# Performance work log

Measured on AMD Instinct MI355X. Metric: run time of the kernel, lower is better.

The kernel has to match this reference:

```python
import jax, jax.numpy as jnp
from jax import lax
import numpy as np

B, W, V, E, H = 512, 40, 12000, 512, 512


def setup_inputs() -> dict:
    key = jax.random.key(0)
    ks = jax.random.split(key, 9)
    s = 0.05
    ques_vec = jax.random.randint(ks[0], (B, W), 0, V + 1)          # token ids, 0 = pad
    ques_len = jax.random.randint(ks[1], (B,), 1, W + 1)             # valid lengths in [1, W]
    lookup_W = jax.random.normal(ks[2], (E, V), jnp.float32) * s     # nn.Linear(vocab, emb).weight
    wih0 = jax.random.normal(ks[3], (2, 4 * H, E), jnp.float32) * s  # [dir, 4H, in]
    whh0 = jax.random.normal(ks[4], (2, 4 * H, H), jnp.float32) * s
    b0 = jax.random.normal(ks[5], (2, 2, 4 * H), jnp.float32) * s    # [dir, {b_ih,b_hh}, 4H]
    wih1 = jax.random.normal(ks[6], (2, 4 * H, 2 * H), jnp.float32) * s
    whh1 = jax.random.normal(ks[7], (2, 4 * H, H), jnp.float32) * s
    b1 = jax.random.normal(ks[8], (2, 2, 4 * H), jnp.float32) * s
    return {"ques_vec": ques_vec, "ques_len": ques_len, "lookup_W": lookup_W,
            "wih0": wih0, "whh0": whh0, "b0": b0,
            "wih1": wih1, "whh1": whh1, "b1": b1}


def _lstm_dir(x, wih, whh, b, reverse):
    # x: [B, T, D]; PyTorch gate order i, f, g, o
    Hc = whh.shape[1]
    xg = jnp.einsum('btd,gd->btg', x, wih) + b[0] + b[1]  # [B, T, 4H]
    xs = jnp.swapaxes(xg, 0, 1)                            # [T, B, 4H]
    if reverse:
        xs = xs[::-1]

    def step(carry, g_t):
        h, c = carry
        g = g_t + h @ whh.T
        i, f, gg, o = jnp.split(g, 4, axis=-1)
        c = jax.nn.sigmoid(f) * c + jax.nn.sigmoid(i) * jnp.tanh(gg)
        h = jax.nn.sigmoid(o) * jnp.tanh(c)
        return (h, c), h

    h0 = jnp.zeros((x.shape[0], Hc), x.dtype)
    _, hs = lax.scan(step, (h0, h0), xs)
    if reverse:
        hs = hs[::-1]
    return jnp.swapaxes(hs, 0, 1)  # [B, T, H]


def _bilstm(x, wih, whh, b):
    fwd = _lstm_dir(x, wih[0], whh[0], b[0], False)
    bwd = _lstm_dir(x, wih[1], whh[1], b[1], True)
    return jnp.concatenate([fwd, bwd], axis=-1)  # [B, T, 2H]


def reference(ques_vec, ques_len, lookup_W, wih0, whh0, b0, wih1, whh1, b1):
    # one-hot over vocab+1 with column 0 dropped == gather with id 0 -> zero vector
    table = jnp.concatenate([jnp.zeros((1, E), lookup_W.dtype), lookup_W.T], axis=0)  # [V+1, E]
    emb = jnp.tanh(table[ques_vec])          # [B, W, E] (dropout=0 -> identity)
    h = _bilstm(emb, wih0, whh0, b0)         # layer 0
    h = _bilstm(h, wih1, whh1, b1)           # layer 1 -> [B, W, 2H]
    # scatter-mask bmm == select hidden state at timestep ques_len-1
    idx = (ques_len - 1)[:, None, None]
    return jnp.take_along_axis(h, idx, axis=1).reshape(ques_vec.shape[0], -1)  # [B, 2H]
```

## Files before the change

### kernel.cpp

```cpp
#include <hip/hip_runtime.h>
#include <hip/hip_bf16.h>
#include <stdint.h>

#define NB 512
#define NW 40
#define NE 512
#define NH 512
#define NV 12000
#define G4 2048

typedef unsigned short u16;
typedef unsigned int u32;
typedef unsigned long long u64;
typedef __attribute__((ext_vector_type(8))) short short8;
typedef __attribute__((ext_vector_type(4))) float f32x4;

__device__ __forceinline__ unsigned short f2bf(float f) {
  unsigned int u = __float_as_uint(f);
  u += 0x7FFF + ((u >> 16) & 1);
  return (unsigned short)(u >> 16);
}
__device__ __forceinline__ float bf2f(unsigned short b) {
  return __uint_as_float(((unsigned int)b) << 16);
}
__device__ __forceinline__ float loadIn(const void* p, long i, int bf) {
  return bf ? bf2f(((const u16*)p)[i]) : ((const float*)p)[i];
}
__device__ __forceinline__ float fast_tanh(float x) {
  float ax = __builtin_fabsf(x);
  float t = 1.f - 2.f * __builtin_amdgcn_rcpf(__expf(ax + ax) + 1.f);
  return __builtin_copysignf(t, x);
}
__device__ __forceinline__ float sigm(float x) {
  return __builtin_amdgcn_rcpf(1.f + __expf(-x));
}

__global__ void detect_kernel(const u16* p, int* flag) {
  __shared__ int cnt;
  int i = threadIdx.x;
  if (i == 0) cnt = 0;
  __syncthreads();
  unsigned short u = p[2 * (i * 1001)];
  int e = (u >> 7) & 0xFF;
  if (e >= 100 && e <= 126) atomicAdd(&cnt, 1);
  __syncthreads();
  if (i == 0) *flag = (cnt >= 32) ? 1 : 0;
}

__global__ void table_kernel(const void* lookup, const int* flag, u16* tableT) {
  __shared__ float tile[64][65];
  int bf = *flag;
  int v0 = blockIdx.x * 64, e0 = blockIdx.y * 64;
  int tx = threadIdx.x, ty = threadIdx.y;
#pragma unroll
  for (int r = 0; r < 16; ++r) {
    int e = r * 4 + ty, v = tx;
    if (v0 + v < NV)
      tile[e][v] = tanhf(loadIn(lookup, (long)(e0 + e) * NV + v0 + v, bf));
  }
  __syncthreads();
#pragma unroll
  for (int r = 0; r < 16; ++r) {
    int v = r * 4 + ty, e = tx;
    if (v0 + v < NV)
      tableT[(long)(v0 + v) * NE + e0 + e] = f2bf(tile[e][v]);
  }
}

__global__ void embed_kernel(const int* __restrict__ qv,
                             const u16* __restrict__ tableT,
                             u16* __restrict__ emb) {
  int tid = blockIdx.x * 256 + threadIdx.x;
  int token = tid >> 6;
  int chunk = tid & 63;
  int tt = token / NB, b = token % NB;
  int q = qv[b * NW + tt];
  uint4 val = make_uint4(0u, 0u, 0u, 0u);
  if (q > 0) val = *(const uint4*)(tableT + (long)(q - 1) * NE + chunk * 8);
  *(uint4*)(emb + (long)token * NE + chunk * 8) = val;
}

__global__ void pack_kernel(const void* wih0, const void* whh0, const void* b0,
                            const void* wih1, const void* whh1, const void* b1,
                            const int* flag, u16* Wc0, u16* Wc1, float* bsum) {
  const long N0 = 2L * G4 * 1024, N1 = 2L * G4 * 1536;
  long idx = (long)blockIdx.x * 256 + threadIdx.x;
  int bf = *flag;
  if (idx < N0) {
    int d = (int)(idx / (G4 * 1024));
    int rem = (int)(idx % (long)(G4 * 1024));
    int g = rem / 1024, k = rem % 1024;
    float v = (k < 512) ? loadIn(wih0, ((long)d * G4 + g) * 512 + k, bf)
                        : loadIn(whh0, ((long)d * G4 + g) * 512 + (k - 512), bf);
    Wc0[idx] = f2bf(v);
  } else if (idx < N0 + N1) {
    long i2 = idx - N0;
    int d = (int)(i2 / (G4 * 1536));
    int rem = (int)(i2 % (long)(G4 * 1536));
    int g = rem / 1536, k = rem % 1536;
    float v = (k < 1024) ? loadIn(wih1, ((long)d * G4 + g) * 1024 + k, bf)
                         : loadIn(whh1, ((long)d * G4 + g) * 512 + (k - 1024), bf);
    Wc1[i2] = f2bf(v);
  } else if (idx < N0 + N1 + 2L * 2 * G4) {
    long i3 = idx - N0 - N1;
    int layer = (int)(i3 / (2 * G4));
    int d = (int)((i3 / G4) & 1);
    int g = (int)(i3 % G4);
    const void* bb = layer ? b1 : b0;
    float v = loadIn(bb, (long)d * 2 * G4 + g, bf) +
              loadIn(bb, (long)d * 2 * G4 + G4 + g, bf);
    bsum[i3] = v;
  }
}

__global__ void zero_bar(unsigned int* bar) {
  bar[blockIdx.x * 256 + threadIdx.x] = 0u;
}

__global__ __launch_bounds__(256, 2) void xg_gemm(
    const u16* __restrict__ X, int Kx, int Kfull, const u16* __restrict__ Wc,
    const float* __restrict__ bsumL, u16* __restrict__ xg) {
  __shared__ __align__(16) char lds[32768];
  const int tid = threadIdx.x;
  const int lane = tid & 63, wv = tid >> 6;
  const int wm = wv & 1, wn = wv >> 1;
  const int col = lane & 15, quad = lane >> 4;
  const int s = blockIdx.x >> 5, w = blockIdx.x & 31;
  const int bx = (s % 40) * 4 + (w & 3);
  const int by = (s / 40) * 8 + (w >> 2);
  const int tb0 = bx * 128;
  const int d = by >> 4, colb = by & 15, j0 = colb * 32;

  f32x4 zero = {0.f, 0.f, 0.f, 0.f};
  f32x4 acc[4][4];
#pragma unroll
  for (int i = 0; i < 4; ++i)
#pragma unroll
    for (int j = 0; j < 4; ++j) acc[i][j] = zero;

  const int iters = Kx >> 6;
  for (int it = 0; it < iters; ++it) {
    int k0 = it << 6;
#pragma unroll
    for (int p = 0; p < 8; ++p) {
      int c = p * 256 + tid;
      const u16* gsrc;
      if (c < 1024) {
        int r = c >> 3, sl = c & 7;
        int kk = k0 + ((sl * 8) ^ ((r & 7) << 3));
        gsrc = X + (long)(tb0 + r) * Kx + kk;
      } else {
        int cb = c - 1024;
        int r = cb >> 3, sl = cb & 7;
        int kk = k0 + ((sl * 8) ^ ((r & 7) << 3));
        int grow = (r >> 5) * 512 + j0 + (r & 31);
        gsrc = Wc + ((long)d * G4 + grow) * Kfull + kk;
      }
      __builtin_amdgcn_global_load_lds(
          (const __attribute__((address_space(1))) void*)(const void*)gsrc,
          (__attribute__((address_space(3))) void*)(lds + p * 4096 + wv * 1024),
          16, 0, 0);
    }
    __syncthreads();
    const u16* As = (const u16*)lds;
    const u16* Bs = (const u16*)(lds + 16384);
#pragma unroll
    for (int ks = 0; ks < 2; ++ks) {
      short8 afr[4], bfr[4];
#pragma unroll
      for (int mf = 0; mf < 4; ++mf) {
        int rm = wm * 64 + mf * 16 + col;
        int sl = (ks * 32 + quad * 8) ^ ((rm & 7) << 3);
        afr[mf] = *(const short8*)(As + rm * 64 + sl);
      }
#pragma unroll
      for (int nf = 0; nf < 4; ++nf) {
        int br = wn * 64 + nf * 16 + col;
        int sl = (ks * 32 + quad * 8) ^ ((br & 7) << 3);
        bfr[nf] = *(const short8*)(Bs + br * 64 + sl);
      }
#pragma unroll
      for (int mf = 0; mf < 4; ++mf)
#pragma unroll
        for (int nf = 0; nf < 4; ++nf)
          acc[mf][nf] = __builtin_amdgcn_mfma_f32_16x16x32_bf16(
              afr[mf], bfr[nf], acc[mf][nf], 0, 0, 0);
    }
    __syncthreads();
  }

  float bias[4];
#pragma unroll
  for (int nf = 0; nf < 4; ++nf) {
    int n = wn * 64 + nf * 16 + col;
    bias[nf] = bsumL[d * G4 + (n >> 5) * 512 + j0 + (n & 31)];
  }
#pragma unroll
  for (int mf = 0; mf < 4; ++mf)
#pragma unroll
    for (int nf = 0; nf < 4; ++nf) {
      int n = wn * 64 + nf * 16 + col;
      int g = n >> 5, jn = n & 31;
#pragma unroll
      for (int r = 0; r < 4; ++r) {
        int m = wm * 64 + mf * 16 + quad * 4 + r;
        int tb = tb0 + m, t = tb >> 9, b = tb & 511;
        long oi = ((((long)t * 2 + d) * 16 + colb) * 512 + b) * 128 + jn * 4 + g;
        xg[oi] = f2bf(acc[mf][nf][r] + bias[nf]);
      }
    }
}

__global__ __launch_bounds__(256, 1) void lstm_pers(
    const u16* __restrict__ xg, const u16* __restrict__ Wc, int Kfull, int Kx,
    u16* __restrict__ hbuf, u16* __restrict__ h0cat, void* __restrict__ outp,
    const int* __restrict__ qlen, const int* __restrict__ flag,
    unsigned int* bar, int layer) {
  __shared__ __align__(16) char lds[163840];
  const int tid = threadIdx.x;
  const int lane = tid & 63, wv = tid >> 6;
  const int wm = wv & 1, wn = wv >> 1;
  const int col = lane & 15, quad = lane >> 4;
  const int l = blockIdx.x;
  const int colid = l & 31, mi = l >> 5;
  const int colb = colid & 15, j0 = colb * 32, d = colid >> 4;
  const int m0 = mi * 64;
  const int gid = l >> 4;

#pragma unroll
  for (int p = 0; p < 32; ++p) {
    int c = p * 256 + tid;
    int row = c >> 6, rem = c & 63;
    int kc = rem >> 3, sl = rem & 7;
    int grow = (row >> 5) * 512 + j0 + (row & 31);
    int gk = Kx + kc * 64 + ((sl * 8) ^ ((row & 7) << 3));
    const u16* gsrc = Wc + ((long)d * G4 + grow) * Kfull + gk;
    __builtin_amdgcn_global_load_lds(
        (const __attribute__((address_space(1))) void*)(const void*)gsrc,
        (__attribute__((address_space(3))) void*)(lds + p * 4096 + wv * 1024),
        16, 0, 0);
  }
  const u16* Bs = (const u16*)lds;
  char* hstg = lds + 131072;
  u16* hLDS = (u16*)hstg;

  float creg[2][4];
#pragma unroll
  for (int i = 0; i < 2; ++i)
#pragma unroll
    for (int r = 0; r < 4; ++r) creg[i][r] = 0.f;
  const int isbf = *flag;
  f32x4 zero = {0.f, 0.f, 0.f, 0.f};

  __syncthreads();

#pragma unroll 1
  for (int t = 0; t < NW; ++t) {
    const int tq = d ? (NW - 1 - t) : t;

    ushort4 xgv[2][4];
    const u16* xgt = xg + ((((long)tq * 2 + d) * 16 + colb) * 512 + m0) * 128;
#pragma unroll
    for (int mf = 0; mf < 2; ++mf)
#pragma unroll
      for (int r = 0; r < 4; ++r) {
        int m = wm * 32 + mf * 16 + quad * 4 + r;
        xgv[mf][r] = *(const ushort4*)(xgt + m * 128 + (wn * 16 + col) * 4);
      }

    f32x4 acc[2][4];
#pragma unroll
    for (int i = 0; i < 2; ++i)
#pragma unroll
      for (int j = 0; j < 4; ++j) acc[i][j] = zero;

    if (t > 0) {
      const u16* hp =
          hbuf + ((t - 1) & 1) * (2L * NB * NH) + ((long)d * NB + m0) * NH;
      auto stageH = [&](int half) {
#pragma unroll
        for (int p = 0; p < 8; ++p) {
          int c = p * 256 + tid;
          int row = c >> 5, slot = c & 31;
          int kk = half * 256 + (slot >> 3) * 64 +
                   (((slot & 7) * 8) ^ ((row & 7) << 3));
          const u16* gsrc = hp + (long)row * NH + kk;
          __builtin_amdgcn_global_load_lds(
              (const __attribute__((address_space(1))) void*)(const void*)gsrc,
              (__attribute__((address_space(3))) void*)(hstg + p * 4096 +
                                                        wv * 1024),
              16, 0, 16 );
        }
      };
      const u16* As = (const u16*)hstg;
#pragma unroll 1
      for (int half = 0; half < 2; ++half) {
        stageH(half);
        __syncthreads();
#pragma unroll
        for (int ks = 0; ks < 8; ++ks) {
          const int ksub = ks * 32 + quad * 8;
          short8 afr[2];
#pragma unroll
          for (int mf = 0; mf < 2; ++mf) {
            int rm = wm * 32 + mf * 16 + col;
            afr[mf] = *(const short8*)(As + rm * 256 + (ksub & ~63) +
                                       ((ksub & 63) ^ ((rm & 7) << 3)));
          }
          const int kc = half * 256 + ksub;
#pragma unroll
          for (int g = 0; g < 4; ++g) {
            int br = g * 32 + wn * 16 + col;
            int slb = (kc & 63) ^ ((br & 7) << 3);
            short8 bfr = *(const short8*)(Bs + br * 512 + (kc & ~63) + slb);
#pragma unroll
            for (int mf = 0; mf < 2; ++mf)
              acc[mf][g] = __builtin_amdgcn_mfma_f32_16x16x32_bf16(
                  afr[mf], bfr, acc[mf][g], 0, 0, 0);
          }
        }
        __syncthreads();
      }
    }

#pragma unroll
    for (int mf = 0; mf < 2; ++mf)
#pragma unroll
      for (int r = 0; r < 4; ++r) {
        int m = wm * 32 + mf * 16 + quad * 4 + r;
        const u16* xv = (const u16*)&xgv[mf][r];
        float gi = acc[mf][0][r] + bf2f(xv[0]);
        float gf = acc[mf][1][r] + bf2f(xv[1]);
        float gg = acc[mf][2][r] + bf2f(xv[2]);
        float go = acc[mf][3][r] + bf2f(xv[3]);
        float si = sigm(gi);
        float sf = sigm(gf);
        float so = sigm(go);
        float cn = sf * creg[mf][r] + si * fast_tanh(gg);
        float h = so * fast_tanh(cn);
        creg[mf][r] = cn;
        hLDS[m * 32 + wn * 16 + col] = f2bf(h);
        if (layer == 1 && !isbf) {
          int bg = m0 + m;
          if (qlen[bg] - 1 == tq)
            ((float*)outp)[(long)bg * (2 * NH) + d * NH + j0 + wn * 16 + col] =
                h;
        }
      }
    __syncthreads();

    u16* hnxt = hbuf + (t & 1) * (2L * NB * NH);
    u32 hw[4];
    int bgp[4], jgp[4];
#pragma unroll
    for (int p = 0; p < 4; ++p) {
      int c = p * 256 + tid;
      int m = c >> 4, pr = c & 15;
      hw[p] = ((const u32*)hLDS)[m * 16 + pr];
      bgp[p] = m0 + m;
      jgp[p] = j0 + pr * 2;
      __hip_atomic_store(
          (u32*)(hnxt + ((long)d * NB + bgp[p]) * NH + jgp[p]), hw[p],
          __ATOMIC_RELAXED, __HIP_MEMORY_SCOPE_AGENT);
    }

    if (t < NW - 1) {
      __syncthreads();
      if (tid == 0) {
        u32* cnt = &bar[gid * 64];
        u32* flg = &bar[1024 + gid * 64];
        unsigned old = __hip_atomic_fetch_add(cnt, 1u, __ATOMIC_RELAXED,
                                              __HIP_MEMORY_SCOPE_AGENT);
        if (old == 16u * (t + 1) - 1u)
          __hip_atomic_store(flg, (unsigned)(t + 1), __ATOMIC_RELAXED,
                             __HIP_MEMORY_SCOPE_AGENT);
        else
          while (__hip_atomic_load(flg, __ATOMIC_RELAXED,
                                   __HIP_MEMORY_SCOPE_AGENT) <
                 (unsigned)(t + 1))
            __builtin_amdgcn_s_sleep(1);
      }
      __syncthreads();
    }

#pragma unroll
    for (int p = 0; p < 4; ++p) {
      if (layer == 0) {
        *(u32*)(h0cat + ((long)tq * NB + bgp[p]) * (2 * NH) + d * NH +
                jgp[p]) = hw[p];
      } else if (isbf && qlen[bgp[p]] - 1 == tq) {
        *(u32*)((u16*)outp + (long)bgp[p] * (2 * NH) + d * NH + jgp[p]) =
            hw[p];
      }
    }
  }
}

extern "C" void kernel_launch(void* const* d_in, const int* in_sizes, int n_in,
                              void* d_out, int out_size, void* d_ws,
                              size_t ws_size, hipStream_t stream) {
  const int* qv = (const int*)d_in[0];
  const int* ql = (const int*)d_in[1];
  const void* lookup = d_in[2];
  const void* wih0 = d_in[3];
  const void* whh0 = d_in[4];
  const void* b0 = d_in[5];
  const void* wih1 = d_in[6];
  const void* whh1 = d_in[7];
  const void* b1 = d_in[8];

  char* ws = (char*)d_ws;
  size_t off = 0;
  int* flag = (int*)ws;                 off += 256;
  unsigned int* bar = (unsigned int*)(ws + off); off += 8192;
  float* bsum = (float*)(ws + off);     off += 2L * 2 * G4 * 4;
  u16* Wc0 = (u16*)(ws + off);          off += 2L * G4 * 1024 * 2;
  u16* Wc1 = (u16*)(ws + off);          off += 2L * G4 * 1536 * 2;
  u16* hbuf = (u16*)(ws + off);         off += 2L * 2 * NB * NH * 2;
  u16* h0cat = (u16*)(ws + off);        off += (size_t)NW * NB * 2 * NH * 2;
  u16* emb = (u16*)(ws + off);          off += (size_t)NW * NB * NE * 2;
  u16* xg = (u16*)(ws + off);           off += (size_t)NW * 2 * 16 * 512 * 128 * 2;
  u16* tableT = h0cat;

  detect_kernel<<<1, 64, 0, stream>>>((const u16*)lookup, flag);
  table_kernel<<<dim3(188, 8), dim3(64, 4), 0, stream>>>(lookup, flag, tableT);
  {
    long total = 2L * G4 * 1024 + 2L * G4 * 1536 + 2L * 2 * G4;
    int blocks = (int)((total + 255) / 256);
    pack_kernel<<<blocks, 256, 0, stream>>>(wih0, whh0, b0, wih1, whh1, b1,
                                            flag, Wc0, Wc1, bsum);
  }
  embed_kernel<<<NW * NB / 4, 256, 0, stream>>>(qv, tableT, emb);

  xg_gemm<<<5120, 256, 0, stream>>>(emb, 512, 1024, Wc0, bsum, xg);
  zero_bar<<<8, 256, 0, stream>>>(bar);
  lstm_pers<<<256, 256, 0, stream>>>(xg, Wc0, 1024, 512, hbuf, h0cat, d_out,
                                     ql, flag, bar, 0);
  xg_gemm<<<5120, 256, 0, stream>>>(h0cat, 1024, 1536, Wc1, bsum + 2 * G4, xg);
  zero_bar<<<8, 256, 0, stream>>>(bar);
  lstm_pers<<<256, 256, 0, stream>>>(xg, Wc1, 1536, 1024, hbuf, h0cat, d_out,
                                     ql, flag, bar, 1);
}
```

Before: 949.2 us.

## Precompute per-vocab layer-0 gate table and replace counter barrier with per-block flags

Layer 0's input projection is computed once per vocabulary entry (12000 rows) instead of once per token (20480 tokens), giving a gate table G indexed by token id. Row 0 holds only the bias, for padding. The LSTM kernel then gathers its precomputed gates through qv, which removes the embed kernel and the emb buffer. The grid barrier changes from a counter plus flag to per-block step flags that one wave polls with a ballot before reading h. The g_gemm tail guards v<NV while the grid covers 94*128 rows. Occupancy for xg_gemm is also bumped from 2 to 3.

```diff
diff --git a/kernel.cpp b/kernel.cpp
--- a/kernel.cpp
+++ b/kernel.cpp
@@ -67,23 +67,12 @@
   }
 }
 
-__global__ void embed_kernel(const int* __restrict__ qv,
-                             const u16* __restrict__ tableT,
-                             u16* __restrict__ emb) {
-  int tid = blockIdx.x * 256 + threadIdx.x;
-  int token = tid >> 6;
-  int chunk = tid & 63;
-  int tt = token / NB, b = token % NB;
-  int q = qv[b * NW + tt];
-  uint4 val = make_uint4(0u, 0u, 0u, 0u);
-  if (q > 0) val = *(const uint4*)(tableT + (long)(q - 1) * NE + chunk * 8);
-  *(uint4*)(emb + (long)token * NE + chunk * 8) = val;
-}
-
 __global__ void pack_kernel(const void* wih0, const void* whh0, const void* b0,
                             const void* wih1, const void* whh1, const void* b1,
-                            const int* flag, u16* Wc0, u16* Wc1, float* bsum) {
+                            const int* flag, u16* Wc0, u16* Wc1, float* bsum,
+                            u16* G) {
   const long N0 = 2L * G4 * 1024, N1 = 2L * G4 * 1536;
+  const long NB2 = 2L * 2 * G4;
   long idx = (long)blockIdx.x * 256 + threadIdx.x;
   int bf = *flag;
   if (idx < N0) {
@@ -101,7 +90,7 @@
     float v = (k < 1024) ? loadIn(wih1, ((long)d * G4 + g) * 1024 + k, bf)
                          : loadIn(whh1, ((long)d * G4 + g) * 512 + (k - 1024), bf);
     Wc1[i2] = f2bf(v);
-  } else if (idx < N0 + N1 + 2L * 2 * G4) {
+  } else if (idx < N0 + N1 + NB2) {
     long i3 = idx - N0 - N1;
     int layer = (int)(i3 / (2 * G4));
     int d = (int)((i3 / G4) & 1);
@@ -110,6 +99,15 @@
     float v = loadIn(bb, (long)d * 2 * G4 + g, bf) +
               loadIn(bb, (long)d * 2 * G4 + G4 + g, bf);
     bsum[i3] = v;
+  } else if (idx < N0 + N1 + NB2 + 4096) {
+    int n = (int)(idx - N0 - N1 - NB2);
+    int d = n >> 11, loc = n & 2047;
+    int colb = loc >> 7, rr = loc & 127;
+    int jn = rr >> 2, g = rr & 3;
+    int grow = g * 512 + colb * 32 + jn;
+    float v = loadIn(b0, (long)d * 2 * G4 + grow, bf) +
+              loadIn(b0, (long)d * 2 * G4 + G4 + grow, bf);
+    G[n] = f2bf(v);
   }
 }
 
@@ -117,7 +115,100 @@
   bar[blockIdx.x * 256 + threadIdx.x] = 0u;
 }
 
-__global__ __launch_bounds__(256, 2) void xg_gemm(
+__global__ __launch_bounds__(256, 3) void g_gemm(
+    const u16* __restrict__ tableT, const u16* __restrict__ Wc,
+    const float* __restrict__ bsumL, u16* __restrict__ G) {
+  __shared__ __align__(16) char lds[32768];
+  const int tid = threadIdx.x;
+  const int lane = tid & 63, wv = tid >> 6;
+  const int wm = wv & 1, wn = wv >> 1;
+  const int col = lane & 15, quad = lane >> 4;
+  const int bx = blockIdx.x >> 5;
+  const int by = blockIdx.x & 31;
+  const int tb0 = bx * 128;
+  const int d = by >> 4, colb = by & 15, j0 = colb * 32;
+
+  f32x4 zero = {0.f, 0.f, 0.f, 0.f};
+  f32x4 acc[4][4];
+#pragma unroll
+  for (int i = 0; i < 4; ++i)
+#pragma unroll
+    for (int j = 0; j < 4; ++j) acc[i][j] = zero;
+
+  for (int it = 0; it < 8; ++it) {
+    int k0 = it << 6;
+#pragma unroll
+    for (int p = 0; p < 8; ++p) {
+      int c = p * 256 + tid;
+      const u16* gsrc;
+      if (c < 1024) {
+        int r = c >> 3, sl = c & 7;
+        int kk = k0 + ((sl * 8) ^ ((r & 7) << 3));
+        gsrc = tableT + (long)(tb0 + r) * 512 + kk;
+      } else {
+        int cb = c - 1024;
+        int r = cb >> 3, sl = cb & 7;
+        int kk = k0 + ((sl * 8) ^ ((r & 7) << 3));
+        int grow = (r >> 5) * 512 + j0 + (r & 31);
+        gsrc = Wc + ((long)d * G4 + grow) * 1024 + kk;
+      }
+      __builtin_amdgcn_global_load_lds(
+          (const __attribute__((address_space(1))) void*)(const void*)gsrc,
+          (__attribute__((address_space(3))) void*)(lds + p * 4096 + wv * 1024),
+          16, 0, 0);
+    }
+    __syncthreads();
+    const u16* As = (const u16*)lds;
+    const u16* Bs = (const u16*)(lds + 16384);
+#pragma unroll
+    for (int ks = 0; ks < 2; ++ks) {
+      short8 afr[4], bfr[4];
+#pragma unroll
+      for (int mf = 0; mf < 4; ++mf) {
+        int rm = wm * 64 + mf * 16 + col;
+        int sl = (ks * 32 + quad * 8) ^ ((rm & 7) << 3);
+        afr[mf] = *(const short8*)(As + rm * 64 + sl);
+      }
+#pragma unroll
+      for (int nf = 0; nf < 4; ++nf) {
+        int br = wn * 64 + nf * 16 + col;
+        int sl = (ks * 32 + quad * 8) ^ ((br & 7) << 3);
+        bfr[nf] = *(const short8*)(Bs + br * 64 + sl);
+      }
+#pragma unroll
+      for (int mf = 0; mf < 4; ++mf)
+#pragma unroll
+        for (int nf = 0; nf < 4; ++nf)
+          acc[mf][nf] = __builtin_amdgcn_mfma_f32_16x16x32_bf16(
+              afr[mf], bfr[nf], acc[mf][nf], 0, 0, 0);
+    }
+    __syncthreads();
+  }
+
+  float bias[4];
+#pragma unroll
+  for (int nf = 0; nf < 4; ++nf) {
+    int n = wn * 64 + nf * 16 + col;
+    bias[nf] = bsumL[d * G4 + (n >> 5) * 512 + j0 + (n & 31)];
+  }
+#pragma unroll
+  for (int mf = 0; mf < 4; ++mf)
+#pragma unroll
+    for (int nf = 0; nf < 4; ++nf) {
+      int n = wn * 64 + nf * 16 + col;
+      int g = n >> 5, jn = n & 31;
+#pragma unroll
+      for (int r = 0; r < 4; ++r) {
+        int m = wm * 64 + mf * 16 + quad * 4 + r;
+        int v = tb0 + m;
+        if (v < NV)
+          G[(long)(v + 1) * 4096 + ((d * 16 + colb) << 7) + jn * 4 + g] =
+              f2bf(acc[mf][nf][r] + bias[nf]);
+      }
+    }
+}
+
+__global__ __launch_bounds__(256, 3) void xg_gemm(
     const u16* __restrict__ X, int Kx, int Kfull, const u16* __restrict__ Wc,
     const float* __restrict__ bsumL, u16* __restrict__ xg) {
   __shared__ __align__(16) char lds[32768];
@@ -212,8 +303,9 @@
 }
 
 __global__ __launch_bounds__(256, 1) void lstm_pers(
-    const u16* __restrict__ xg, const u16* __restrict__ Wc, int Kfull, int Kx,
-    u16* __restrict__ hbuf, u16* __restrict__ h0cat, void* __restrict__ outp,
+    const u16* __restrict__ xg, const int* __restrict__ qv,
+    const u16* __restrict__ Wc, int Kfull, int Kx, u16* __restrict__ hbuf,
+    u16* __restrict__ h0cat, void* __restrict__ outp,
     const int* __restrict__ qlen, const int* __restrict__ flag,
     unsigned int* bar, int layer) {
   __shared__ __align__(16) char lds[163840];
@@ -259,14 +351,28 @@
     const int tq = d ? (NW - 1 - t) : t;
 
     ushort4 xgv[2][4];
-    const u16* xgt = xg + ((((long)tq * 2 + d) * 16 + colb) * 512 + m0) * 128;
-#pragma unroll
-    for (int mf = 0; mf < 2; ++mf)
-#pragma unroll
-      for (int r = 0; r < 4; ++r) {
-        int m = wm * 32 + mf * 16 + quad * 4 + r;
-        xgv[mf][r] = *(const ushort4*)(xgt + m * 128 + (wn * 16 + col) * 4);
-      }
+    if (layer == 0) {
+#pragma unroll
+      for (int mf = 0; mf < 2; ++mf)
+#pragma unroll
+        for (int r = 0; r < 4; ++r) {
+          int m = wm * 32 + mf * 16 + quad * 4 + r;
+          int q = qv[(m0 + m) * NW + tq];
+          xgv[mf][r] = *(const ushort4*)(xg + (long)q * 4096 +
+                                         ((d * 16 + colb) << 7) +
+                                         (wn * 16 + col) * 4);
+        }
+    } else {
+      const u16* xgt =
+          xg + ((((long)tq * 2 + d) * 16 + colb) * 512 + m0) * 128;
+#pragma unroll
+      for (int mf = 0; mf < 2; ++mf)
+#pragma unroll
+        for (int r = 0; r < 4; ++r) {
+          int m = wm * 32 + mf * 16 + quad * 4 + r;
+          xgv[mf][r] = *(const ushort4*)(xgt + m * 128 + (wn * 16 + col) * 4);
+        }
+    }
 
     f32x4 acc[2][4];
 #pragma unroll
@@ -275,6 +381,15 @@
       for (int j = 0; j < 4; ++j) acc[i][j] = zero;
 
     if (t > 0) {
+      if (wv == 0) {
+        u32* sp = bar + gid * 16 + (lane & 15);
+        while (__ballot((int)(__hip_atomic_load(sp, __ATOMIC_RELAXED,
+                                                __HIP_MEMORY_SCOPE_AGENT) <
+                              (u32)t)))
+          __builtin_amdgcn_s_sleep(1);
+      }
+      __syncthreads();
+
       const u16* hp =
           hbuf + ((t - 1) & 1) * (2L * NB * NH) + ((long)d * NB + m0) * NH;
       auto stageH = [&](int half) {
@@ -366,21 +481,9 @@
 
     if (t < NW - 1) {
       __syncthreads();
-      if (tid == 0) {
-        u32* cnt = &bar[gid * 64];
-        u32* flg = &bar[1024 + gid * 64];
-        unsigned old = __hip_atomic_fetch_add(cnt, 1u, __ATOMIC_RELAXED,
-                                              __HIP_MEMORY_SCOPE_AGENT);
-        if (old == 16u * (t + 1) - 1u)
-          __hip_atomic_store(flg, (unsigned)(t + 1), __ATOMIC_RELAXED,
-                             __HIP_MEMORY_SCOPE_AGENT);
-        else
-          while (__hip_atomic_load(flg, __ATOMIC_RELAXED,
-                                   __HIP_MEMORY_SCOPE_AGENT) <
-                 (unsigned)(t + 1))
-            __builtin_amdgcn_s_sleep(1);
-      }
-      __syncthreads();
+      if (tid == 0)
+        __hip_atomic_store(bar + gid * 16 + colb, (u32)(t + 1),
+                           __ATOMIC_RELAXED, __HIP_MEMORY_SCOPE_AGENT);
     }
 
 #pragma unroll
@@ -418,26 +521,25 @@
   u16* Wc1 = (u16*)(ws + off);          off += 2L * G4 * 1536 * 2;
   u16* hbuf = (u16*)(ws + off);         off += 2L * 2 * NB * NH * 2;
   u16* h0cat = (u16*)(ws + off);        off += (size_t)NW * NB * 2 * NH * 2;
-  u16* emb = (u16*)(ws + off);          off += (size_t)NW * NB * NE * 2;
   u16* xg = (u16*)(ws + off);           off += (size_t)NW * 2 * 16 * 512 * 128 * 2;
   u16* tableT = h0cat;
+  u16* G = xg;
 
   detect_kernel<<<1, 64, 0, stream>>>((const u16*)lookup, flag);
   table_kernel<<<dim3(188, 8), dim3(64, 4), 0, stream>>>(lookup, flag, tableT);
   {
-    long total = 2L * G4 * 1024 + 2L * G4 * 1536 + 2L * 2 * G4;
+    long total = 2L * G4 * 1024 + 2L * G4 * 1536 + 2L * 2 * G4 + 4096;
     int blocks = (int)((total + 255) / 256);
     pack_kernel<<<blocks, 256, 0, stream>>>(wih0, whh0, b0, wih1, whh1, b1,
-                                            flag, Wc0, Wc1, bsum);
-  }
-  embed_kernel<<<NW * NB / 4, 256, 0, stream>>>(qv, tableT, emb);
-
-  xg_gemm<<<5120, 256, 0, stream>>>(emb, 512, 1024, Wc0, bsum, xg);
+                                            flag, Wc0, Wc1, bsum, G);
+  }
+
+  g_gemm<<<94 * 32, 256, 0, stream>>>(tableT, Wc0, bsum, G);
   zero_bar<<<8, 256, 0, stream>>>(bar);
-  lstm_pers<<<256, 256, 0, stream>>>(xg, Wc0, 1024, 512, hbuf, h0cat, d_out,
-                                     ql, flag, bar, 0);
+  lstm_pers<<<256, 256, 0, stream>>>(G, qv, Wc0, 1024, 512, hbuf, h0cat,
+                                     d_out, ql, flag, bar, 0);
   xg_gemm<<<5120, 256, 0, stream>>>(h0cat, 1024, 1536, Wc1, bsum + 2 * G4, xg);
   zero_bar<<<8, 256, 0, stream>>>(bar);
-  lstm_pers<<<256, 256, 0, stream>>>(xg, Wc1, 1536, 1024, hbuf, h0cat, d_out,
-                                     ql, flag, bar, 1);
-}
+  lstm_pers<<<256, 256, 0, stream>>>(xg, qv, Wc1, 1536, 1024, hbuf, h0cat,
+                                     d_out, ql, flag, bar, 1);
+}
```

New measurement: 853.6 us. -10.1%, faster.
